# Kernel optimization log

Hardware: AMD Instinct MI355X
Metric: run time of the kernel (lower is better)

Reference implementation:

```python
import jax, jax.numpy as jnp
import numpy as np

N, E, DIN, H, C = 50000, 800000, 256, 128, 8


def setup_inputs() -> dict:
    key = jax.random.key(0)
    k1, k2, k3, k4 = jax.random.split(key, 4)
    x = jax.random.normal(k1, (N, DIN), dtype=jnp.float32)
    edge_index = jax.random.randint(k2, (2, E), 0, N, dtype=jnp.int64)
    W1 = jax.random.normal(k3, (DIN, H), dtype=jnp.float32) * (1.0 / np.sqrt(DIN))
    b1 = jnp.zeros((H,), dtype=jnp.float32)
    W2 = jax.random.normal(k4, (H, C), dtype=jnp.float32) * (1.0 / np.sqrt(H))
    b2 = jnp.zeros((C,), dtype=jnp.float32)
    return {"x": x, "W1": W1, "b1": b1, "W2": W2, "b2": b2, "edge_index": edge_index}


def reference(x, W1, b1, W2, b2, edge_index):
    n = x.shape[0]
    loop = jnp.arange(n, dtype=edge_index.dtype)
    src = jnp.concatenate([edge_index[0], loop])  # messages flow src -> dst
    dst = jnp.concatenate([edge_index[1], loop])
    # symmetric GCN normalization with self-loops (PyG GCNConv default)
    deg = jax.ops.segment_sum(jnp.ones_like(dst, dtype=x.dtype), dst, num_segments=n)
    dinv = jnp.where(deg > 0, deg ** -0.5, 0.0)
    norm = dinv[src] * dinv[dst]  # [E+N]

    def gcn_layer(h, W, b):
        h = h @ W                                   # [N, d_out]
        msg = norm[:, None] * h[src]                # gather: [E+N, d_out]
        agg = jax.ops.segment_sum(msg, dst, num_segments=n)  # scatter-add
        return agg + b

    h = jax.nn.relu(gcn_layer(x, W1, b1))
    # F.dropout(training=False) is identity in eval mode
    out = gcn_layer(h, W2, b2)
    return jax.nn.log_softmax(out, axis=1)
```

## Files before the change

kernel.cpp:

```cpp
#include <hip/hip_runtime.h>
#include <hip/hip_bf16.h>
#include <stdint.h>

#define DIN 256
#define HD  128
#define CD  8
#define KCH 64
#define SBW 72
#define CSRW 64

typedef __attribute__((ext_vector_type(8))) short bf16x8;
typedef __attribute__((ext_vector_type(4))) float f32x4;

__device__ __forceinline__ float bf2f(unsigned short u) {
    union { unsigned int i; float f; } v; v.i = ((unsigned int)u) << 16; return v.f;
}
__device__ __forceinline__ unsigned short f2bf(float f) {
    union { float f; unsigned int i; } v; v.f = f;
    unsigned int r = v.i + 0x7fffu + ((v.i >> 16) & 1u);
    return (unsigned short)(r >> 16);
}
__device__ __forceinline__ int edge_at(const void* ei, int is64, long long idx) {
    return is64 ? (int)((const long long*)ei)[idx] : ((const int*)ei)[idx];
}

__global__ __launch_bounds__(256) void prep_kernel(
    const float* __restrict__ W1, unsigned short* __restrict__ W1T,
    int* __restrict__ count, int N)
{
    int tg = blockIdx.x * 256 + threadIdx.x;
    if (tg < HD * (DIN / 4)) {
        int n  = tg & (HD - 1);
        int k4 = (tg >> 7) * 4;
        unsigned short v[4];
#pragma unroll
        for (int j = 0; j < 4; j++) v[j] = f2bf(W1[(k4 + j) * HD + n]);
        *reinterpret_cast<unsigned long long*>(W1T + (size_t)n * DIN + k4) =
            ((unsigned long long)v[0]) | ((unsigned long long)v[1] << 16) |
            ((unsigned long long)v[2] << 32) | ((unsigned long long)v[3] << 48);
    }
    for (int i = tg; i < N; i += 256 * 256) count[i] = 0;
}

__global__ __launch_bounds__(256) void gemm1_scatter_kernel(
    const float* __restrict__ x, const unsigned short* __restrict__ W1T,
    unsigned short* __restrict__ h, int M,
    const void* __restrict__ ei,
    int* __restrict__ count, unsigned short* __restrict__ colf, int E, int N, int G1)
{
    __shared__ unsigned short w1t[HD * SBW];
    if ((int)blockIdx.x >= G1) {
        const int lane = threadIdx.x & 63;
        int oddw = ((const int*)ei)[2 * lane + 1];
        unsigned long long zb = __ballot(oddw == 0);
        int is64 = (__popcll(zb) >= 56) ? 1 : 0;
        int e0 = ((int)blockIdx.x - G1) * 512 + threadIdx.x;
#pragma unroll
        for (int k = 0; k < 2; k++) {
            int e = e0 + k * 256;
            if (e < E) {
                int s = edge_at(ei, is64, e);
                int d = edge_at(ei, is64, (long long)E + e);
                if ((unsigned)d < (unsigned)N && (unsigned)s < (unsigned)N) {
                    int slot = atomicAdd(&count[d], 1);
                    if (slot < CSRW)
                        colf[(d << 6) + slot] = (unsigned short)s;
                }
            }
        }
        return;
    }
    const int tid  = threadIdx.x;
    const int lane = tid & 63;
    const int wave = tid >> 6;
    const int quad = lane >> 4;
    const int r15  = lane & 15;
    const long long rowBase = (long long)blockIdx.x * 128 + wave * 32;

    f32x4 acc[2][8];
#pragma unroll
    for (int rt = 0; rt < 2; rt++)
#pragma unroll
        for (int ct = 0; ct < 8; ct++)
#pragma unroll
            for (int i = 0; i < 4; i++) acc[rt][ct][i] = 0.0f;

    for (int kh = 0; kh < DIN / KCH; kh++) {
        __syncthreads();
        for (int c = tid; c < HD * (KCH / 8); c += 256) {
            int n   = c >> 3;
            int kk0 = (c & 7) * 8;
            bf16x8 v = *reinterpret_cast<const bf16x8*>(W1T + (size_t)n * DIN + kh * KCH + kk0);
            *reinterpret_cast<bf16x8*>(&w1t[n * SBW + kk0]) = v;
        }
        __syncthreads();

        for (int ki = 0; ki < KCH / 32; ki++) {
            int kk0 = ki * 32 + quad * 8;
            int kg  = kh * KCH + kk0;
            bf16x8 a[2];
#pragma unroll
            for (int rt = 0; rt < 2; rt++) {
                long long row = rowBase + rt * 16 + r15;
                if (row < M) {
                    const float* xp = x + row * DIN + kg;
                    f32x4 f0 = *reinterpret_cast<const f32x4*>(xp);
                    f32x4 f1 = *reinterpret_cast<const f32x4*>(xp + 4);
#pragma unroll
                    for (int j = 0; j < 4; j++) {
                        a[rt][j]     = (short)f2bf(f0[j]);
                        a[rt][j + 4] = (short)f2bf(f1[j]);
                    }
                } else {
#pragma unroll
                    for (int j = 0; j < 8; j++) a[rt][j] = 0;
                }
            }
#pragma unroll
            for (int ct = 0; ct < 8; ct++) {
                bf16x8 b = *reinterpret_cast<const bf16x8*>(&w1t[(ct * 16 + r15) * SBW + kk0]);
                acc[0][ct] = __builtin_amdgcn_mfma_f32_16x16x32_bf16(a[0], b, acc[0][ct], 0, 0, 0);
                acc[1][ct] = __builtin_amdgcn_mfma_f32_16x16x32_bf16(a[1], b, acc[1][ct], 0, 0, 0);
            }
        }
    }
#pragma unroll
    for (int rt = 0; rt < 2; rt++)
#pragma unroll
        for (int ct = 0; ct < 8; ct++)
#pragma unroll
            for (int i = 0; i < 4; i++) {
                long long row = rowBase + rt * 16 + quad * 4 + i;
                if (row < M) h[row * HD + ct * 16 + r15] = f2bf(acc[rt][ct][i]);
            }
}

__global__ __launch_bounds__(256) void agg1_fused_kernel(
    const unsigned short* __restrict__ h, const int* __restrict__ count,
    const unsigned short* __restrict__ colf, const float* __restrict__ b1,
    const float* __restrict__ W2, float* __restrict__ hw2, int N)
{
    const int lane = threadIdx.x & 63;
    const int n = blockIdx.x * 4 + (threadIdx.x >> 6);
    if (n >= N) return;

    float w2a[CD], w2b[CD];
#pragma unroll
    for (int c = 0; c < CD; c++) {
        w2a[c] = W2[(2 * lane)     * CD + c];
        w2b[c] = W2[(2 * lane + 1) * CD + c];
    }

    int deg = count[n]; if (deg > CSRW) deg = CSRW;
    const float dn = rsqrtf((float)deg + 1.0f);
    union U2 { unsigned int u; unsigned short s[2]; };
    U2 p; p.u = *reinterpret_cast<const unsigned int*>(h + (size_t)n * HD + 2 * lane);
    float acc0 = dn * dn * bf2f(p.s[0]);
    float acc1 = dn * dn * bf2f(p.s[1]);

    const int base = n << 6;
    int i = 0;
    for (; i + 7 < deg; i += 8) {
        unsigned long long c0 = *reinterpret_cast<const unsigned long long*>(colf + base + i);
        unsigned long long c1 = *reinterpret_cast<const unsigned long long*>(colf + base + i + 4);
        int s[8];
#pragma unroll
        for (int j = 0; j < 4; j++) {
            s[j]     = (int)((c0 >> (16 * j)) & 0xFFFFu);
            s[j + 4] = (int)((c1 >> (16 * j)) & 0xFFFFu);
        }
        int d[8];
#pragma unroll
        for (int j = 0; j < 8; j++) d[j] = count[s[j]];
        U2 hv[8];
#pragma unroll
        for (int j = 0; j < 8; j++)
            hv[j].u = *reinterpret_cast<const unsigned int*>(h + (size_t)s[j] * HD + 2 * lane);
        float g[8];
#pragma unroll
        for (int j = 0; j < 8; j++)
            g[j] = rsqrtf((float)min(d[j], CSRW) + 1.0f) * dn;
#pragma unroll
        for (int j = 0; j < 8; j++) {
            acc0 += g[j] * bf2f(hv[j].s[0]);
            acc1 += g[j] * bf2f(hv[j].s[1]);
        }
    }
    for (; i < deg; i++) {
        int s0 = colf[base + i];
        float g0 = rsqrtf((float)min(count[s0], CSRW) + 1.0f) * dn;
        U2 a; a.u = *reinterpret_cast<const unsigned int*>(h + (size_t)s0 * HD + 2 * lane);
        acc0 += g0 * bf2f(a.s[0]);
        acc1 += g0 * bf2f(a.s[1]);
    }

    float v0 = acc0 + b1[2 * lane];     v0 = v0 > 0.0f ? v0 : 0.0f;
    float v1 = acc1 + b1[2 * lane + 1]; v1 = v1 > 0.0f ? v1 : 0.0f;

    float part[CD];
#pragma unroll
    for (int c = 0; c < CD; c++) part[c] = v0 * w2a[c] + v1 * w2b[c];
#pragma unroll
    for (int m = 1; m < 64; m <<= 1)
#pragma unroll
        for (int c = 0; c < CD; c++) part[c] += __shfl_xor(part[c], m, 64);
    if (lane < CD) hw2[(size_t)n * CD + lane] = dn * part[lane];
}

__global__ void agg2_kernel(const float* __restrict__ hw2, const int* __restrict__ count,
                            const unsigned short* __restrict__ colf, const float* __restrict__ b2,
                            float* __restrict__ out, int N) {
    int g = blockIdx.x * 256 + threadIdx.x;
    bool act = g < N * CD;
    int n = act ? (g >> 3) : 0;
    int c = g & 7;
    int deg = count[n]; if (deg > CSRW) deg = CSRW;
    float dn = rsqrtf((float)deg + 1.0f);
    float acc = hw2[(size_t)n * CD + c];
    const int base = n << 6;
    for (int i = 0; i < deg; i++) {
        int s = colf[base + i];
        acc += hw2[(size_t)s * CD + c];
    }
    acc = dn * acc + b2[c];
    float mx = acc;
#pragma unroll
    for (int m = 1; m < 8; m <<= 1) mx = fmaxf(mx, __shfl_xor(mx, m, 64));
    float ex = expf(acc - mx);
    float s8 = ex;
#pragma unroll
    for (int m = 1; m < 8; m <<= 1) s8 += __shfl_xor(s8, m, 64);
    float res = (acc - mx) - logf(s8);
    if (act) out[g] = res;
}

extern "C" void kernel_launch(void* const* d_in, const int* in_sizes, int n_in,
                              void* d_out, int out_size, void* d_ws, size_t ws_size,
                              hipStream_t stream) {
    const float* x  = (const float*)d_in[0];
    const float* W1 = (const float*)d_in[1];
    const float* b1 = (const float*)d_in[2];
    const float* W2 = (const float*)d_in[3];
    const float* b2 = (const float*)d_in[4];
    const void*  ei = d_in[5];
    const int N = in_sizes[0] / DIN;
    const int E = in_sizes[5] / 2;
    const int G1 = (N + 127) / 128;
    const int G2 = (E + 511) / 512;

    char* ws = (char*)d_ws;
    size_t off = 0;
    auto alloc = [&](size_t bytes) -> void* {
        void* p = ws + off;
        off = (off + bytes + 255) & ~(size_t)255;
        return p;
    };
    int*   count = (int*)alloc((size_t)N * 4);
    unsigned short* colf = (unsigned short*)alloc((size_t)N * CSRW * 2);
    unsigned short* h = (unsigned short*)alloc((size_t)N * HD * 2);
    float* hw2 = (float*)alloc((size_t)N * CD * 4);
    unsigned short* W1T = (unsigned short*)alloc((size_t)HD * DIN * 2);

    prep_kernel         <<<256, 256, 0, stream>>>(W1, W1T, count, N);
    gemm1_scatter_kernel<<<G1 + G2, 256, 0, stream>>>(x, W1T, h, N, ei, count, colf, E, N, G1);
    agg1_fused_kernel   <<<(N + 3) / 4, 256, 0, stream>>>(h, count, colf, b1, W2, hw2, N);
    agg2_kernel         <<<(N * CD + 255) / 256, 256, 0, stream>>>(hw2, count, colf, b2,
                                                                   (float*)d_out, N);
}
```

Before: 208.1 us.

## Prescale GEMM1 rows by source norm into fp16 buffer before aggregation

Adds a scale_kernel that multiplies each row of h by its node's inverse-sqrt degree and stores it as fp16. Aggregation then gathers prescaled rows and applies the destination norm once, dropping the per-edge count gather and rsqrt. The cross-lane reduction of the 8 class partials is also replaced by a recursive-halving exchange that uses fewer shuffles. The cost is an extra kernel launch plus a read and write of the full h matrix, and fp16 storage trades mantissa for range relative to bf16.

```diff
diff --git a/kernel.cpp b/kernel.cpp
--- a/kernel.cpp
+++ b/kernel.cpp
@@ -1,5 +1,6 @@
 #include <hip/hip_runtime.h>
 #include <hip/hip_bf16.h>
+#include <hip/hip_fp16.h>
 #include <stdint.h>
 
 #define DIN 256
@@ -135,8 +136,28 @@
             }
 }
 
+__global__ __launch_bounds__(256) void scale_kernel(
+    const unsigned short* __restrict__ h, const int* __restrict__ count,
+    unsigned short* __restrict__ h2, int N)
+{
+    int t = blockIdx.x * 256 + threadIdx.x;
+    if (t >= N * (HD / 8)) return;
+    int n = t >> 4;
+    int deg = count[n]; if (deg > CSRW) deg = CSRW;
+    float dn = rsqrtf((float)deg + 1.0f);
+    bf16x8 v = *reinterpret_cast<const bf16x8*>(h + (size_t)t * 8);
+    bf16x8 o;
+#pragma unroll
+    for (int j = 0; j < 8; j++) {
+        float f = bf2f((unsigned short)v[j]) * dn;
+        __half hf = __float2half(f);
+        o[j] = *reinterpret_cast<short*>(&hf);
+    }
+    *reinterpret_cast<bf16x8*>(h2 + (size_t)t * 8) = o;
+}
+
 __global__ __launch_bounds__(256) void agg1_fused_kernel(
-    const unsigned short* __restrict__ h, const int* __restrict__ count,
+    const unsigned short* __restrict__ h2, const int* __restrict__ count,
     const unsigned short* __restrict__ colf, const float* __restrict__ b1,
     const float* __restrict__ W2, float* __restrict__ hw2, int N)
 {
@@ -153,58 +174,82 @@
 
     int deg = count[n]; if (deg > CSRW) deg = CSRW;
     const float dn = rsqrtf((float)deg + 1.0f);
-    union U2 { unsigned int u; unsigned short s[2]; };
-    U2 p; p.u = *reinterpret_cast<const unsigned int*>(h + (size_t)n * HD + 2 * lane);
-    float acc0 = dn * dn * bf2f(p.s[0]);
-    float acc1 = dn * dn * bf2f(p.s[1]);
+
+    union UH { unsigned int u; __half2 h; };
+    UH p; p.u = *reinterpret_cast<const unsigned int*>(h2 + ((size_t)n << 7) + 2 * lane);
+    float2 pf = __half22float2(p.h);
+    float acc0 = pf.x, acc1 = pf.y;
 
     const int base = n << 6;
     int i = 0;
     for (; i + 7 < deg; i += 8) {
         unsigned long long c0 = *reinterpret_cast<const unsigned long long*>(colf + base + i);
         unsigned long long c1 = *reinterpret_cast<const unsigned long long*>(colf + base + i + 4);
-        int s[8];
+        unsigned int s[8];
 #pragma unroll
         for (int j = 0; j < 4; j++) {
-            s[j]     = (int)((c0 >> (16 * j)) & 0xFFFFu);
-            s[j + 4] = (int)((c1 >> (16 * j)) & 0xFFFFu);
-        }
-        int d[8];
-#pragma unroll
-        for (int j = 0; j < 8; j++) d[j] = count[s[j]];
-        U2 hv[8];
+            s[j]     = (unsigned int)((c0 >> (16 * j)) & 0xFFFFu);
+            s[j + 4] = (unsigned int)((c1 >> (16 * j)) & 0xFFFFu);
+        }
+        UH hv[8];
 #pragma unroll
         for (int j = 0; j < 8; j++)
-            hv[j].u = *reinterpret_cast<const unsigned int*>(h + (size_t)s[j] * HD + 2 * lane);
-        float g[8];
-#pragma unroll
-        for (int j = 0; j < 8; j++)
-            g[j] = rsqrtf((float)min(d[j], CSRW) + 1.0f) * dn;
+            hv[j].u = *reinterpret_cast<const unsigned int*>(h2 + ((size_t)s[j] << 7) + 2 * lane);
 #pragma unroll
         for (int j = 0; j < 8; j++) {
-            acc0 += g[j] * bf2f(hv[j].s[0]);
-            acc1 += g[j] * bf2f(hv[j].s[1]);
+            float2 f = __half22float2(hv[j].h);
+            acc0 += f.x;
+            acc1 += f.y;
         }
     }
     for (; i < deg; i++) {
-        int s0 = colf[base + i];
-        float g0 = rsqrtf((float)min(count[s0], CSRW) + 1.0f) * dn;
-        U2 a; a.u = *reinterpret_cast<const unsigned int*>(h + (size_t)s0 * HD + 2 * lane);
-        acc0 += g0 * bf2f(a.s[0]);
-        acc1 += g0 * bf2f(a.s[1]);
-    }
-
-    float v0 = acc0 + b1[2 * lane];     v0 = v0 > 0.0f ? v0 : 0.0f;
-    float v1 = acc1 + b1[2 * lane + 1]; v1 = v1 > 0.0f ? v1 : 0.0f;
+        unsigned int s0 = colf[base + i];
+        UH a; a.u = *reinterpret_cast<const unsigned int*>(h2 + ((size_t)s0 << 7) + 2 * lane);
+        float2 f = __half22float2(a.h);
+        acc0 += f.x;
+        acc1 += f.y;
+    }
+
+    float v0 = dn * acc0 + b1[2 * lane];     v0 = v0 > 0.0f ? v0 : 0.0f;
+    float v1 = dn * acc1 + b1[2 * lane + 1]; v1 = v1 > 0.0f ? v1 : 0.0f;
 
     float part[CD];
 #pragma unroll
     for (int c = 0; c < CD; c++) part[c] = v0 * w2a[c] + v1 * w2b[c];
-#pragma unroll
-    for (int m = 1; m < 64; m <<= 1)
-#pragma unroll
-        for (int c = 0; c < CD; c++) part[c] += __shfl_xor(part[c], m, 64);
-    if (lane < CD) hw2[(size_t)n * CD + lane] = dn * part[lane];
+
+    float t4[4];
+    {
+        int hi = lane & 1;
+#pragma unroll
+        for (int k = 0; k < 4; k++) {
+            float send = hi ? part[k] : part[4 + k];
+            float recv = __shfl_xor(send, 1, 64);
+            t4[k] = (hi ? part[4 + k] : part[k]) + recv;
+        }
+    }
+    float t2[2];
+    {
+        int hi = (lane >> 1) & 1;
+#pragma unroll
+        for (int k = 0; k < 2; k++) {
+            float send = hi ? t2[0] * 0.0f + t4[k] : t4[2 + k];
+            send = hi ? t4[k] : t4[2 + k];
+            float recv = __shfl_xor(send, 2, 64);
+            t2[k] = (hi ? t4[2 + k] : t4[k]) + recv;
+        }
+    }
+    float t1;
+    {
+        int hi = (lane >> 2) & 1;
+        float send = hi ? t2[0] : t2[1];
+        float recv = __shfl_xor(send, 4, 64);
+        t1 = (hi ? t2[1] : t2[0]) + recv;
+    }
+    t1 += __shfl_xor(t1, 8, 64);
+    t1 += __shfl_xor(t1, 16, 64);
+    t1 += __shfl_xor(t1, 32, 64);
+    int c = ((lane & 1) << 2) | (lane & 2) | ((lane >> 2) & 1);
+    if (lane < CD) hw2[(size_t)n * CD + c] = dn * t1;
 }
 
 __global__ void agg2_kernel(const float* __restrict__ hw2, const int* __restrict__ count,
@@ -258,12 +303,14 @@
     int*   count = (int*)alloc((size_t)N * 4);
     unsigned short* colf = (unsigned short*)alloc((size_t)N * CSRW * 2);
     unsigned short* h = (unsigned short*)alloc((size_t)N * HD * 2);
+    unsigned short* h2 = (unsigned short*)alloc((size_t)N * HD * 2);
     float* hw2 = (float*)alloc((size_t)N * CD * 4);
     unsigned short* W1T = (unsigned short*)alloc((size_t)HD * DIN * 2);
 
     prep_kernel         <<<256, 256, 0, stream>>>(W1, W1T, count, N);
     gemm1_scatter_kernel<<<G1 + G2, 256, 0, stream>>>(x, W1T, h, N, ei, count, colf, E, N, G1);
-    agg1_fused_kernel   <<<(N + 3) / 4, 256, 0, stream>>>(h, count, colf, b1, W2, hw2, N);
+    scale_kernel        <<<(N * (HD / 8) + 255) / 256, 256, 0, stream>>>(h, count, h2, N);
+    agg1_fused_kernel   <<<(N + 3) / 4, 256, 0, stream>>>(h2, count, colf, b1, W2, hw2, N);
     agg2_kernel         <<<(N * CD + 255) / 256, 256, 0, stream>>>(hw2, count, colf, b2,
                                                                    (float*)d_out, N);
 }
```

After: 202.1 us. -2.9%, faster.
